# Performance work log

Measured on AMD Instinct MI355X. Metric: run time of the kernel, lower is better.

## Reference

```python
import jax, jax.numpy as jnp
import numpy as np

N_NODES = 100000
N_EDGES = 3200000
D_IN = 128
HEADS = 8
F_OUT = 64


def setup_inputs() -> dict:
    key = jax.random.key(0)
    k1, k2, k3, k4, k5, k6 = jax.random.split(key, 6)
    node_features = jax.random.normal(k1, (N_NODES, D_IN), dtype=jnp.float32)
    linear_proj = jax.random.normal(k2, (D_IN, HEADS * F_OUT), dtype=jnp.float32) * (1.0 / np.sqrt(D_IN))
    scoring_fn_source = jax.random.normal(k3, (1, HEADS, F_OUT), dtype=jnp.float32) * 0.1
    scoring_fn_target = jax.random.normal(k4, (1, HEADS, F_OUT), dtype=jnp.float32) * 0.1
    edge_index = jax.random.randint(k5, (2, N_EDGES), 0, N_NODES, dtype=jnp.int64)
    return {
        'node_features': node_features,
        'linear_proj': linear_proj,
        'scoring_fn_source': scoring_fn_source,
        'scoring_fn_target': scoring_fn_target,
        'edge_index': edge_index,
    }


def reference(node_features, linear_proj, scoring_fn_source, scoring_fn_target, edge_index):
    # node_features: [N, D_in]; edge_index: [2, E] (row 0 = src, row 1 = trg)
    N = node_features.shape[0]
    H, F = scoring_fn_source.shape[1], scoring_fn_source.shape[2]

    # linear projection: [N, H, F]
    proj = (node_features @ linear_proj).reshape(N, H, F)

    # per-node attention scores: [N, H]
    scores_source = jnp.sum(proj * scoring_fn_source, axis=-1)
    scores_target = jnp.sum(proj * scoring_fn_target, axis=-1)

    src, trg = edge_index[0], edge_index[1]
    # lift to edges + LeakyReLU: [E, H]
    scores_per_edge = jax.nn.leaky_relu(scores_source[src] + scores_target[trg],
                                        negative_slope=0.2)

    # neighborhood-aware softmax over edges sharing the same target node
    seg_max = jax.ops.segment_max(scores_per_edge, trg, num_segments=N)   # [N, H]
    exp_scores = jnp.exp(scores_per_edge - seg_max[trg])                  # [E, H]
    seg_sum = jax.ops.segment_sum(exp_scores, trg, num_segments=N)        # [N, H]
    attentions_per_edge = exp_scores / (seg_sum[trg] + 1e-16)             # [E, H]
    return attentions_per_edge
```

## Files before the change

kernel.cpp:

```cpp
#include <hip/hip_runtime.h>
#include <hip/hip_fp16.h>

#define D_IN   128
#define HEADS  8
#define FOUT   64
#define NOUT   16
#define NPB    512
#define NPB_SH 9
#define NB_MAX 1024
#define CHUNK  8192
#define NBLK_MAX 1024
#define TPN    8
#define SROWS  64
#define SPAD   129
#define DET_BLOCKS 128

typedef unsigned __attribute__((ext_vector_type(2))) uint2v;
typedef float    __attribute__((ext_vector_type(4))) float4v;

__device__ __forceinline__ unsigned pack2(float a, float b) {
    union { __half2 h; unsigned u; } c;
    c.h = __floats2half2_rn(a, b);
    return c.u;
}
__device__ __forceinline__ float2 up2(unsigned u) {
    union { unsigned x; __half2 h; } c;
    c.x = u;
    return __half22float2(c.h);
}

__device__ __forceinline__ unsigned ntl_u(const unsigned* p) {
    return __builtin_nontemporal_load(p);
}
__device__ __forceinline__ uint2v ntl_u2(const unsigned* p) {
    return __builtin_nontemporal_load((const uint2v*)p);
}
__device__ __forceinline__ float4v ntl_f4(const float* p) {
    return __builtin_nontemporal_load((const float4v*)p);
}
__device__ __forceinline__ void nts_f4(float* p, float4v v) {
    __builtin_nontemporal_store(v, (float4v*)p);
}

__device__ __forceinline__ void load_edge(const unsigned int* idx, int e, int E,
                                          bool is64, unsigned int& s, unsigned int& t) {
    if (is64) {
        uint2v a = ntl_u2(idx + 2 * (size_t)e);
        uint2v b = ntl_u2(idx + 2 * ((size_t)E + e));
        s = a.x; t = b.x;
    } else {
        s = ntl_u(idx + e);
        t = ntl_u(idx + (size_t)E + e);
    }
}

__device__ __forceinline__ unsigned int load_trg(const unsigned int* idx, int e, int E,
                                                 bool is64) {
    if (is64) { uint2v b = ntl_u2(idx + 2 * ((size_t)E + e)); return b.x; }
    return ntl_u(idx + (size_t)E + e);
}

__global__ void k_fold_w(const float* __restrict__ W,
                         const float* __restrict__ a_src,
                         const float* __restrict__ a_trg,
                         float* __restrict__ Wc,
                         unsigned int* __restrict__ flag,
                         int* __restrict__ binTotal, int NB) {
    int t = blockIdx.x * blockDim.x + threadIdx.x;
    if (t == 0) *flag = 0u;
    if (t < NB) binTotal[t] = 0;
    if (t >= D_IN * HEADS) return;
    int d = t >> 3, h = t & 7;
    const float* wrow = W + d * (HEADS * FOUT) + h * FOUT;
    float s1 = 0.f, s2 = 0.f;
    #pragma unroll 4
    for (int f = 0; f < FOUT; ++f) {
        float w = wrow[f];
        s1 += w * a_src[h * FOUT + f];
        s2 += w * a_trg[h * FOUT + f];
    }
    Wc[h * D_IN + d]           = s1;
    Wc[(HEADS + h) * D_IN + d] = s2;
}

__global__ void k_scores_t(const float* __restrict__ x,
                           const float* __restrict__ Wc,
                           float* __restrict__ ssrc_f,
                           float* __restrict__ strg_f,
                           __half* __restrict__ ssrc_h, int N,
                           const unsigned int* __restrict__ idx_w, int dwords,
                           unsigned int* __restrict__ flag) {
    if (blockIdx.x < DET_BLOCKS) {
        unsigned int local = 0;
        int stride = DET_BLOCKS * 256;
        for (int i = blockIdx.x * 256 + threadIdx.x; 2 * i + 1 < dwords; i += stride)
            local |= idx_w[2 * i + 1];
        if (__any(local != 0) && (threadIdx.x & 63) == 0)
            atomicOr(flag, 1u);
    }

    __shared__ float xt[SROWS * SPAD];
    int node0 = blockIdx.x * SROWS;
    int tid   = threadIdx.x;
    int nrows = min(SROWS, N - node0);

    for (int i = tid; i < nrows * 32; i += 256) {
        int r = i >> 5, c = (i & 31) * 4;
        float4v v = ntl_f4(x + (size_t)(node0 + r) * D_IN + c);
        float* dst = &xt[r * SPAD + c];
        dst[0] = v.x; dst[1] = v.y; dst[2] = v.z; dst[3] = v.w;
    }
    __syncthreads();

    int r  = tid & 63;
    int og = tid >> 6;
    if (r >= nrows) return;
    int n = node0 + r;

    const float* w = Wc + og * 4 * D_IN;
    float a0 = 0.f, a1 = 0.f, a2 = 0.f, a3 = 0.f;
    const float* xr = &xt[r * SPAD];
    #pragma unroll 8
    for (int d = 0; d < D_IN; ++d) {
        float xv = xr[d];
        a0 += xv * w[d];
        a1 += xv * w[D_IN + d];
        a2 += xv * w[2 * D_IN + d];
        a3 += xv * w[3 * D_IN + d];
    }

    float4 res = make_float4(a0, a1, a2, a3);
    if (og < 2) *(float4*)(ssrc_f + (size_t)n * HEADS + og * 4)       = res;
    else        *(float4*)(strg_f + (size_t)n * HEADS + (og - 2) * 4) = res;
    if (og < 2) {
        uint2 hp;
        hp.x = pack2(a0, a1);
        hp.y = pack2(a2, a3);
        *(uint2*)(ssrc_h + (size_t)n * HEADS + og * 4) = hp;
    }
}

__global__ void k_hist(const unsigned int* __restrict__ idx, int E,
                       const unsigned int* __restrict__ flag,
                       int* __restrict__ histB, int NB, int NBLK,
                       int* __restrict__ binTotal) {
    __shared__ int h[NB_MAX];
    for (int i = threadIdx.x; i < NB; i += blockDim.x) h[i] = 0;
    __syncthreads();
    bool is64 = (*flag == 0u);
    int base = blockIdx.x * CHUNK;
    int lim  = min(base + CHUNK, E);
    for (int e = base + threadIdx.x; e < lim; e += blockDim.x) {
        unsigned int t = load_trg(idx, e, E, is64);
        atomicAdd(&h[t >> NPB_SH], 1);
    }
    __syncthreads();
    for (int i = threadIdx.x; i < NB; i += blockDim.x) {
        histB[(size_t)i * NBLK + blockIdx.x] = h[i];
        if (h[i]) atomicAdd(&binTotal[i], h[i]);
    }
}

__global__ void k_scan(const int* __restrict__ histB,
                       int* __restrict__ histA, int NB, int NBLK,
                       const int* __restrict__ binTotal,
                       int* __restrict__ binBase) {
    int b = blockIdx.x;
    int tid = threadIdx.x;
    if (b < NB) {
        __shared__ int v[NBLK_MAX];
        v[tid] = (tid < NBLK) ? histB[(size_t)b * NBLK + tid] : 0;
        __syncthreads();
        for (int off = 1; off < NBLK_MAX; off <<= 1) {
            int t = (tid >= off) ? v[tid - off] : 0;
            __syncthreads();
            v[tid] += t;
            __syncthreads();
        }
        if (tid < NBLK)
            histA[(size_t)tid * NB + b] = tid ? v[tid - 1] : 0;
    } else {
        __shared__ int v[NB_MAX];
        v[tid] = (tid < NB) ? binTotal[tid] : 0;
        __syncthreads();
        for (int off = 1; off < NB_MAX; off <<= 1) {
            int t = (tid >= off) ? v[tid - off] : 0;
            __syncthreads();
            v[tid] += t;
            __syncthreads();
        }
        if (tid < NB)
            binBase[tid] = tid ? v[tid - 1] : 0;
    }
}

__global__ void k_scatter(const unsigned int* __restrict__ idx, int E,
                          const unsigned int* __restrict__ flag,
                          const int* __restrict__ histA, int NB,
                          const int* __restrict__ binBase,
                          unsigned int* __restrict__ binned) {
    __shared__ int cnt[NB_MAX];
    for (int i = threadIdx.x; i < NB; i += blockDim.x)
        cnt[i] = binBase[i] + histA[(size_t)blockIdx.x * NB + i];
    __syncthreads();
    bool is64 = (*flag == 0u);
    int base = blockIdx.x * CHUNK;
    int lim  = min(base + CHUNK, E);
    for (int e = base + threadIdx.x; e < lim; e += blockDim.x) {
        unsigned int s, t;
        load_edge(idx, e, E, is64, s, t);
        int pos = atomicAdd(&cnt[t >> NPB_SH], 1);
        binned[pos] = s | ((t & (NPB - 1u)) << 20);
    }
}

__global__ void k_sortsum(const unsigned int* __restrict__ binned,
                          const int* __restrict__ binBase,
                          const int* __restrict__ binTotal,
                          const __half* __restrict__ ssrc_h,
                          const float* __restrict__ strg_f,
                          unsigned int* __restrict__ sortedSrc,
                          __half* __restrict__ combo, int N, int NB) {
    __shared__ int cnt[NPB];
    __shared__ int scn[NPB];
    __shared__ int off[NPB];
    int b = blockIdx.x;
    int node0 = b << NPB_SH;
    int start = binBase[b], total = binTotal[b];
    int i = threadIdx.x;

    cnt[i] = 0;
    __syncthreads();
    for (int e = i; e < total; e += NPB)
        atomicAdd(&cnt[binned[start + e] >> 20], 1);
    __syncthreads();

    scn[i] = cnt[i];
    __syncthreads();
    for (int o = 1; o < NPB; o <<= 1) {
        int t = (i >= o) ? scn[i - o] : 0;
        __syncthreads();
        scn[i] += t;
        __syncthreads();
    }
    off[i] = scn[i] - cnt[i];
    cnt[i] = off[i];
    __syncthreads();

    for (int e = i; e < total; e += NPB) {
        unsigned int v = binned[start + e];
        int pos = atomicAdd(&cnt[v >> 20], 1);
        sortedSrc[start + pos] = v & 0xFFFFFu;
    }
    __threadfence_block();
    __syncthreads();

    int k  = i & (TPN - 1);
    int lg = i >> 3;
    for (int l = lg; l < NPB; l += NPB / TPN) {
        int n = node0 + l;
        if (n >= N) break;
        int r0 = start + off[l];
        int r1 = start + scn[l];

        const float4* tp = (const float4*)(strg_f + (size_t)n * HEADS);
        float4 ta = tp[0], tb = tp[1];
        float st[8] = { ta.x, ta.y, ta.z, ta.w, tb.x, tb.y, tb.z, tb.w };
        float acc[8] = { 0, 0, 0, 0, 0, 0, 0, 0 };

        for (int e = r0 + k; e < r1; e += TPN) {
            unsigned int s = sortedSrc[e];
            uint4 sv = *(const uint4*)(ssrc_h + (size_t)s * HEADS);
            float2 f01 = up2(sv.x), f23 = up2(sv.y), f45 = up2(sv.z), f67 = up2(sv.w);
            float vs[8] = { f01.x, f01.y, f23.x, f23.y, f45.x, f45.y, f67.x, f67.y };
            #pragma unroll
            for (int h = 0; h < HEADS; ++h) {
                float sc = vs[h] + st[h];
                sc = sc > 0.f ? sc : 0.2f * sc;
                acc[h] += expf(sc);
            }
        }
        #pragma unroll
        for (int h = 0; h < HEADS; ++h) {
            acc[h] += __shfl_xor(acc[h], 1, 64);
            acc[h] += __shfl_xor(acc[h], 2, 64);
            acc[h] += __shfl_xor(acc[h], 4, 64);
        }
        if (k == 0) {
            float rs[8];
            #pragma unroll
            for (int h = 0; h < HEADS; ++h) rs[h] = 1.0f / (acc[h] + 1e-16f);
            uint4 c0, c1;
            c0.x = pack2(st[0], st[1]);  c0.y = pack2(st[2], st[3]);
            c0.z = pack2(st[4], st[5]);  c0.w = pack2(st[6], st[7]);
            c1.x = pack2(rs[0], rs[1]);  c1.y = pack2(rs[2], rs[3]);
            c1.z = pack2(rs[4], rs[5]);  c1.w = pack2(rs[6], rs[7]);
            uint4* cp = (uint4*)(combo + (size_t)n * 16);
            cp[0] = c0;
            cp[1] = c1;
        }
    }
}

__global__ void k_edge_out_c(const unsigned int* __restrict__ idx, int E,
                             const __half* __restrict__ ssrc_h,
                             const __half* __restrict__ combo,
                             const unsigned int* __restrict__ flag,
                             float* __restrict__ out) {
    int e = blockIdx.x * blockDim.x + threadIdx.x;
    if (e >= E) return;
    bool is64 = (*flag == 0u);
    unsigned int s, t;
    load_edge(idx, e, E, is64, s, t);

    uint4 sv = *(const uint4*)(ssrc_h + (size_t)s * HEADS);
    const uint4* cp = (const uint4*)(combo + (size_t)t * 16);
    uint4 c0 = cp[0], c1 = cp[1];

    float2 s01 = up2(sv.x), s23 = up2(sv.y), s45 = up2(sv.z), s67 = up2(sv.w);
    float2 t01 = up2(c0.x), t23 = up2(c0.y), t45 = up2(c0.z), t67 = up2(c0.w);
    float2 r01 = up2(c1.x), r23 = up2(c1.y), r45 = up2(c1.z), r67 = up2(c1.w);

    float ss[8] = { s01.x, s01.y, s23.x, s23.y, s45.x, s45.y, s67.x, s67.y };
    float st[8] = { t01.x, t01.y, t23.x, t23.y, t45.x, t45.y, t67.x, t67.y };
    float rs[8] = { r01.x, r01.y, r23.x, r23.y, r45.x, r45.y, r67.x, r67.y };

    float o[8];
    #pragma unroll
    for (int h = 0; h < HEADS; ++h) {
        float sc = ss[h] + st[h];
        sc = sc > 0.f ? sc : 0.2f * sc;
        o[h] = expf(sc) * rs[h];
    }
    float4v o0 = { o[0], o[1], o[2], o[3] };
    float4v o1 = { o[4], o[5], o[6], o[7] };
    nts_f4(out + (size_t)e * HEADS,     o0);
    nts_f4(out + (size_t)e * HEADS + 4, o1);
}

__device__ __forceinline__ void edge_scores(const float* ssrc, const float* strg,
                                            unsigned int s, unsigned int t, float* ex) {
    const float4* sp = (const float4*)(ssrc + (size_t)s * HEADS);
    const float4* tp = (const float4*)(strg + (size_t)t * HEADS);
    float4 sa = sp[0], sb = sp[1], ta = tp[0], tb = tp[1];
    float v[8] = { sa.x + ta.x, sa.y + ta.y, sa.z + ta.z, sa.w + ta.w,
                   sb.x + tb.x, sb.y + tb.y, sb.z + tb.z, sb.w + tb.w };
    #pragma unroll
    for (int h = 0; h < HEADS; ++h) {
        float sc = v[h];
        sc = sc > 0.f ? sc : 0.2f * sc;
        ex[h] = expf(sc);
    }
}

__global__ void k_detect_fb(const unsigned int* __restrict__ idx_w, int nwords,
                            unsigned int* __restrict__ flag) {
    unsigned int local = 0;
    int stride = gridDim.x * blockDim.x;
    for (int i = blockIdx.x * blockDim.x + threadIdx.x; 2 * i + 1 < nwords; i += stride)
        local |= idx_w[2 * i + 1];
    if (__any(local != 0) && (threadIdx.x & 63) == 0)
        atomicOr(flag, 1u);
}

__global__ void k_edge_sum(const unsigned int* __restrict__ idx, int E,
                           const float* __restrict__ ssrc,
                           const float* __restrict__ strg,
                           float* __restrict__ sums,
                           const unsigned int* __restrict__ flag) {
    int e = blockIdx.x * blockDim.x + threadIdx.x;
    if (e >= E) return;
    bool is64 = (*flag == 0u);
    unsigned int s, t;
    load_edge(idx, e, E, is64, s, t);
    float ex[8];
    edge_scores(ssrc, strg, s, t, ex);
    float* dst = sums + (size_t)t * HEADS;
    #pragma unroll
    for (int h = 0; h < HEADS; ++h)
        atomicAdd(dst + h, ex[h]);
}

__global__ void k_edge_out(const unsigned int* __restrict__ idx, int E,
                           const float* __restrict__ ssrc,
                           const float* __restrict__ strg,
                           const float* __restrict__ sums,
                           const unsigned int* __restrict__ flag,
                           float* __restrict__ out) {
    int e = blockIdx.x * blockDim.x + threadIdx.x;
    if (e >= E) return;
    bool is64 = (*flag == 0u);
    unsigned int s, t;
    load_edge(idx, e, E, is64, s, t);
    float ex[8];
    edge_scores(ssrc, strg, s, t, ex);
    const float4* sm = (const float4*)(sums + (size_t)t * HEADS);
    float4 m0 = sm[0], m1 = sm[1];
    float4 o0, o1;
    o0.x = ex[0] / (m0.x + 1e-16f);  o0.y = ex[1] / (m0.y + 1e-16f);
    o0.z = ex[2] / (m0.z + 1e-16f);  o0.w = ex[3] / (m0.w + 1e-16f);
    o1.x = ex[4] / (m1.x + 1e-16f);  o1.y = ex[5] / (m1.y + 1e-16f);
    o1.z = ex[6] / (m1.z + 1e-16f);  o1.w = ex[7] / (m1.w + 1e-16f);
    float4* op = (float4*)(out + (size_t)e * HEADS);
    op[0] = o0;
    op[1] = o1;
}

extern "C" void kernel_launch(void* const* d_in, const int* in_sizes, int n_in,
                              void* d_out, int out_size, void* d_ws, size_t ws_size,
                              hipStream_t stream) {
    const float*        x     = (const float*)d_in[0];
    const float*        W     = (const float*)d_in[1];
    const float*        a_src = (const float*)d_in[2];
    const float*        a_trg = (const float*)d_in[3];
    const unsigned int* idx   = (const unsigned int*)d_in[4];

    const int N  = in_sizes[0] / D_IN;
    const int E  = in_sizes[4] / 2;
    const int NH = N * HEADS;
    const int NB   = (N + NPB - 1) / NPB;
    const int NBLK = (E + CHUNK - 1) / CHUNK;

    float* out = (float*)d_out;

    char*  ws  = (char*)d_ws;
    size_t off = 0;
    auto alloc = [&](size_t bytes) { size_t o = off; off = (off + bytes + 255) & ~(size_t)255; return o; };
    size_t NHb = (size_t)NH * sizeof(float);
    float*        sums     = (float*)(ws + alloc(NHb));
    unsigned int* flag     = (unsigned int*)(ws + alloc(4));
    float*        ssrc_f   = (float*)(ws + alloc(NHb));
    float*        strg_f   = (float*)(ws + alloc(NHb));
    __half*       ssrc_h   = (__half*)(ws + alloc((size_t)NH * sizeof(__half)));
    __half*       combo    = (__half*)(ws + alloc((size_t)N * 16 * sizeof(__half)));
    float*        Wc       = (float*)(ws + alloc(NOUT * D_IN * sizeof(float)));
    int*          histA    = (int*)(ws + alloc((size_t)NBLK * NB * sizeof(int)));
    int*          histB    = (int*)(ws + alloc((size_t)NB * NBLK * sizeof(int)));
    int*          binTotal = (int*)(ws + alloc((size_t)NB * sizeof(int)));
    int*          binBase  = (int*)(ws + alloc((size_t)NB * sizeof(int)));
    unsigned int* binned   = (unsigned int*)(ws + alloc((size_t)E * sizeof(unsigned int)));
    unsigned int* sortedS  = (unsigned int*)(ws + alloc((size_t)E * sizeof(unsigned int)));

    const bool fast = (off <= ws_size) && (NB <= NB_MAX) && (NBLK <= NBLK_MAX)
                      && (N < (1 << 20));

    int dwords = in_sizes[4];
    if (dwords > (1 << 20)) dwords = 1 << 20;

    k_fold_w <<<(D_IN * HEADS + 255) / 256, 256, 0, stream>>>(W, a_src, a_trg, Wc,
                                                              flag, binTotal, NB);

    if (fast) {
        k_scores_t <<<(N + SROWS - 1) / SROWS, 256, 0, stream>>>(x, Wc, ssrc_f, strg_f,
                                                                 ssrc_h, N,
                                                                 idx, dwords, flag);
        k_hist    <<<NBLK, 512, 0, stream>>>(idx, E, flag, histB, NB, NBLK, binTotal);
        k_scan    <<<NB + 1, NBLK_MAX, 0, stream>>>(histB, histA, NB, NBLK,
                                                    binTotal, binBase);
        k_scatter <<<NBLK, 512, 0, stream>>>(idx, E, flag, histA, NB, binBase, binned);
        k_sortsum <<<NB, NPB, 0, stream>>>(binned, binBase, binTotal, ssrc_h, strg_f,
                                           sortedS, combo, N, NB);
        k_edge_out_c <<<(E + 255) / 256, 256, 0, stream>>>(idx, E, ssrc_h, combo,
                                                           flag, out);
    } else {
        hipMemsetAsync(sums, 0, NHb, stream);
        k_detect_fb <<<128, 256, 0, stream>>>(idx, dwords, flag);
        k_scores_t <<<(N + SROWS - 1) / SROWS, 256, 0, stream>>>(x, Wc, ssrc_f, strg_f,
                                                                 ssrc_h, N,
                                                                 idx, 0, flag);
        int eblocks = (E + 255) / 256;
        k_edge_sum <<<eblocks, 256, 0, stream>>>(idx, E, ssrc_f, strg_f, sums, flag);
        k_edge_out <<<eblocks, 256, 0, stream>>>(idx, E, ssrc_f, strg_f, sums, flag, out);
    }
}
```

Measured before the change: 238.9 us.

## Split bin sort and per-node softmax sum into separate kernels via row pointers

The fused sort-and-sum kernel is split in two. One kernel sorts sources within each bin and writes a CSR row pointer array. A separate kernel, launched with a grid over all nodes, computes the per-node exp sums and reciprocals. This is meant to avoid the low parallelism of one block per bin (about 196 blocks) during the gather-heavy sum phase. In exchange it adds a kernel launch, a write and read of the row pointers, and a second pass over the sorted sources.

```diff
diff --git a/kernel.cpp b/kernel.cpp
--- a/kernel.cpp
+++ b/kernel.cpp
@@ -214,16 +214,13 @@
     }
 }
 
-__global__ void k_sortsum(const unsigned int* __restrict__ binned,
-                          const int* __restrict__ binBase,
-                          const int* __restrict__ binTotal,
-                          const __half* __restrict__ ssrc_h,
-                          const float* __restrict__ strg_f,
-                          unsigned int* __restrict__ sortedSrc,
-                          __half* __restrict__ combo, int N, int NB) {
+__global__ void k_sort2(const unsigned int* __restrict__ binned,
+                        const int* __restrict__ binBase,
+                        const int* __restrict__ binTotal,
+                        unsigned int* __restrict__ sortedSrc,
+                        int* __restrict__ rowPtr, int N, int NB) {
     __shared__ int cnt[NPB];
     __shared__ int scn[NPB];
-    __shared__ int off[NPB];
     int b = blockIdx.x;
     int node0 = b << NPB_SH;
     int start = binBase[b], total = binTotal[b];
@@ -243,8 +240,13 @@
         scn[i] += t;
         __syncthreads();
     }
-    off[i] = scn[i] - cnt[i];
-    cnt[i] = off[i];
+    {
+        int excl = scn[i] - cnt[i];
+        cnt[i] = excl;
+        int n = node0 + i;
+        if (n < N) rowPtr[n] = start + excl;
+    }
+    if (b == NB - 1 && i == 0) rowPtr[N] = start + total;
     __syncthreads();
 
     for (int e = i; e < total; e += NPB) {
@@ -252,53 +254,54 @@
         int pos = atomicAdd(&cnt[v >> 20], 1);
         sortedSrc[start + pos] = v & 0xFFFFFu;
     }
-    __threadfence_block();
-    __syncthreads();
-
-    int k  = i & (TPN - 1);
-    int lg = i >> 3;
-    for (int l = lg; l < NPB; l += NPB / TPN) {
-        int n = node0 + l;
-        if (n >= N) break;
-        int r0 = start + off[l];
-        int r1 = start + scn[l];
-
-        const float4* tp = (const float4*)(strg_f + (size_t)n * HEADS);
-        float4 ta = tp[0], tb = tp[1];
-        float st[8] = { ta.x, ta.y, ta.z, ta.w, tb.x, tb.y, tb.z, tb.w };
-        float acc[8] = { 0, 0, 0, 0, 0, 0, 0, 0 };
-
-        for (int e = r0 + k; e < r1; e += TPN) {
-            unsigned int s = sortedSrc[e];
-            uint4 sv = *(const uint4*)(ssrc_h + (size_t)s * HEADS);
-            float2 f01 = up2(sv.x), f23 = up2(sv.y), f45 = up2(sv.z), f67 = up2(sv.w);
-            float vs[8] = { f01.x, f01.y, f23.x, f23.y, f45.x, f45.y, f67.x, f67.y };
-            #pragma unroll
-            for (int h = 0; h < HEADS; ++h) {
-                float sc = vs[h] + st[h];
-                sc = sc > 0.f ? sc : 0.2f * sc;
-                acc[h] += expf(sc);
-            }
-        }
+}
+
+__global__ void k_nodesum(const unsigned int* __restrict__ sortedSrc,
+                          const int* __restrict__ rowPtr,
+                          const __half* __restrict__ ssrc_h,
+                          const float* __restrict__ strg_f,
+                          __half* __restrict__ combo, int N) {
+    int gt = blockIdx.x * blockDim.x + threadIdx.x;
+    int n  = gt >> 3;
+    int k  = gt & (TPN - 1);
+    if (n >= N) return;
+
+    int r0 = rowPtr[n], r1 = rowPtr[n + 1];
+    const float4* tp = (const float4*)(strg_f + (size_t)n * HEADS);
+    float4 ta = tp[0], tb = tp[1];
+    float st[8] = { ta.x, ta.y, ta.z, ta.w, tb.x, tb.y, tb.z, tb.w };
+    float acc[8] = { 0, 0, 0, 0, 0, 0, 0, 0 };
+
+    for (int e = r0 + k; e < r1; e += TPN) {
+        unsigned int s = sortedSrc[e];
+        uint4 sv = *(const uint4*)(ssrc_h + (size_t)s * HEADS);
+        float2 f01 = up2(sv.x), f23 = up2(sv.y), f45 = up2(sv.z), f67 = up2(sv.w);
+        float vs[8] = { f01.x, f01.y, f23.x, f23.y, f45.x, f45.y, f67.x, f67.y };
         #pragma unroll
         for (int h = 0; h < HEADS; ++h) {
-            acc[h] += __shfl_xor(acc[h], 1, 64);
-            acc[h] += __shfl_xor(acc[h], 2, 64);
-            acc[h] += __shfl_xor(acc[h], 4, 64);
+            float sc = vs[h] + st[h];
+            sc = sc > 0.f ? sc : 0.2f * sc;
+            acc[h] += expf(sc);
         }
-        if (k == 0) {
-            float rs[8];
-            #pragma unroll
-            for (int h = 0; h < HEADS; ++h) rs[h] = 1.0f / (acc[h] + 1e-16f);
-            uint4 c0, c1;
-            c0.x = pack2(st[0], st[1]);  c0.y = pack2(st[2], st[3]);
-            c0.z = pack2(st[4], st[5]);  c0.w = pack2(st[6], st[7]);
-            c1.x = pack2(rs[0], rs[1]);  c1.y = pack2(rs[2], rs[3]);
-            c1.z = pack2(rs[4], rs[5]);  c1.w = pack2(rs[6], rs[7]);
-            uint4* cp = (uint4*)(combo + (size_t)n * 16);
-            cp[0] = c0;
-            cp[1] = c1;
-        }
+    }
+    #pragma unroll
+    for (int h = 0; h < HEADS; ++h) {
+        acc[h] += __shfl_xor(acc[h], 1, 64);
+        acc[h] += __shfl_xor(acc[h], 2, 64);
+        acc[h] += __shfl_xor(acc[h], 4, 64);
+    }
+    if (k == 0) {
+        float rs[8];
+        #pragma unroll
+        for (int h = 0; h < HEADS; ++h) rs[h] = 1.0f / (acc[h] + 1e-16f);
+        uint4 c0, c1;
+        c0.x = pack2(st[0], st[1]);  c0.y = pack2(st[2], st[3]);
+        c0.z = pack2(st[4], st[5]);  c0.w = pack2(st[6], st[7]);
+        c1.x = pack2(rs[0], rs[1]);  c1.y = pack2(rs[2], rs[3]);
+        c1.z = pack2(rs[4], rs[5]);  c1.w = pack2(rs[6], rs[7]);
+        uint4* cp = (uint4*)(combo + (size_t)n * 16);
+        cp[0] = c0;
+        cp[1] = c1;
     }
 }
 
@@ -440,6 +443,7 @@
     int*          binBase  = (int*)(ws + alloc((size_t)NB * sizeof(int)));
     unsigned int* binned   = (unsigned int*)(ws + alloc((size_t)E * sizeof(unsigned int)));
     unsigned int* sortedS  = (unsigned int*)(ws + alloc((size_t)E * sizeof(unsigned int)));
+    int*          rowPtr   = (int*)(ws + alloc((size_t)(N + 1) * sizeof(int)));
 
     const bool fast = (off <= ws_size) && (NB <= NB_MAX) && (NBLK <= NBLK_MAX)
                       && (N < (1 << 20));
@@ -458,8 +462,11 @@
         k_scan    <<<NB + 1, NBLK_MAX, 0, stream>>>(histB, histA, NB, NBLK,
                                                     binTotal, binBase);
         k_scatter <<<NBLK, 512, 0, stream>>>(idx, E, flag, histA, NB, binBase, binned);
-        k_sortsum <<<NB, NPB, 0, stream>>>(binned, binBase, binTotal, ssrc_h, strg_f,
-                                           sortedS, combo, N, NB);
+        k_sort2   <<<NB, NPB, 0, stream>>>(binned, binBase, binTotal, sortedS,
+                                           rowPtr, N, NB);
+        k_nodesum <<<(N * TPN + 511) / 512, 512, 0, stream>>>(sortedS, rowPtr,
+                                                              ssrc_h, strg_f,
+                                                              combo, N);
         k_edge_out_c <<<(E + 255) / 256, 256, 0, stream>>>(idx, E, ssrc_h, combo,
                                                            flag, out);
     } else {
```

New measurement: 226.1 us. 1.06x faster.
